# Optimization experiments

Measured on AMD Instinct MI355X. Metric: run time of the kernel, lower is better.

Reference implementation:

```python
import jax, jax.numpy as jnp
import numpy as np

NUM_SPIXELS = 256
N_ITER = 3
TEMP = 1.0


def setup_inputs() -> dict:
    key = jax.random.key(0)
    features = jax.random.normal(key, (4, 16, 256, 256), dtype=jnp.float32)
    return {"features": features}


def reference(features):
    B, C, H, W = features.shape
    dt = features.dtype
    # torch.linspace(0, h-1, h)/h == arange(h)/h
    y = jnp.arange(H, dtype=dt) / H
    x = jnp.arange(W, dtype=dt) / W
    mesh_y, mesh_x = jnp.meshgrid(y, x, indexing='ij')  # each [H, W]
    xy = jnp.stack([mesh_x, mesh_y], axis=0)            # [2, H, W]
    xy_b = jnp.broadcast_to(xy, (B, 2, H, W))

    pixel = jnp.concatenate([features, xy_b], axis=1).reshape(B, C + 2, H * W)
    p = pixel.transpose(0, 2, 1)  # [B, N, D], D = C+2

    s = max(1, int(NUM_SPIXELS ** 0.5))
    # adaptive_avg_pool2d to (s, s); H, W divisible by s -> exact block mean
    def pool(t):
        D = t.shape[1]
        return t.reshape(B, D, s, H // s, s, W // s).mean(axis=(3, 5)).reshape(B, D, s * s)

    centers = jnp.concatenate([pool(features), pool(xy_b)], axis=1)  # [B, D, M]
    c = centers.transpose(0, 2, 1)  # [B, M, D]

    Q = None
    for i in range(N_ITER):
        # Euclidean cdist: ||p||^2 + ||c||^2 - 2 p.c, clipped and sqrt'ed
        d2 = (jnp.sum(p * p, axis=-1)[:, :, None]
              + jnp.sum(c * c, axis=-1)[:, None, :]
              - 2.0 * jnp.einsum('bnd,bmd->bnm', p, c))
        dist = jnp.sqrt(jnp.maximum(d2, 1e-12))  # [B, N, M]
        Q = jax.nn.softmax(-dist * TEMP, axis=-1)
        if i < N_ITER - 1:
            norm = jnp.sum(Q, axis=1)[:, :, None] + 1e-6        # [B, M, 1]
            c = jnp.einsum('bnm,bnd->bmd', Q, p) / norm         # [B, M, D]

    centers_feat = c[:, :, :C].transpose(0, 2, 1)  # [B, C, M]
    return Q, centers_feat
```

## Files before the change

### kernel.cpp

```cpp
#include <hip/hip_runtime.h>
#include <hip/hip_bf16.h>
#include <math.h>

#define BB 4
#define CC 16
#define HH 256
#define WW 256
#define NN (HH*WW)
#define MM 256
#define CROW 20
#define PROW 20
#define PIX 32
#define TSUB 4
#define PIXPERBLK (PIX*TSUB)
#define CHUNKS (NN/PIXPERBLK)

typedef float f32x2 __attribute__((ext_vector_type(2)));
typedef float f32x4v __attribute__((ext_vector_type(4)));
typedef short bf16x8 __attribute__((ext_vector_type(8)));

__device__ __forceinline__ f32x2 mk2(float a, float b) { f32x2 r; r.x = a; r.y = b; return r; }
__device__ __forceinline__ f32x2 pk_fma(f32x2 a, f32x2 b, f32x2 c) {
    return __builtin_elementwise_fma(a, b, c);
}

__device__ __forceinline__ short bfhi(float f, float& hif) {
    __hip_bfloat16 h = __float2bfloat16(f);
    hif = __bfloat162float(h);
    return __builtin_bit_cast(short, h);
}
__device__ __forceinline__ short bflo(float f, float hif) {
    __hip_bfloat16 l = __float2bfloat16(f - hif);
    return __builtin_bit_cast(short, l);
}

__global__ void init_centers(const float* __restrict__ feat, float* __restrict__ cbuf)
{
    const int b    = blockIdx.x >> 8;
    const int m    = blockIdx.x & 255;
    const int lane = threadIdx.x;
    const int sy = m >> 4, sx = m & 15;

    float cvals[16];
#pragma unroll
    for (int d = 0; d < 16; ++d) {
        float v = 0.f;
#pragma unroll
        for (int k = 0; k < 4; ++k) {
            int q  = lane + (k << 6);
            int py = q >> 4, px = q & 15;
            int n  = (sy*16 + py)*WW + sx*16 + px;
            v += feat[((b*CC + d) << 16) + n];
        }
#pragma unroll
        for (int off = 32; off; off >>= 1) v += __shfl_down(v, off);
        cvals[d] = v * (1.f/256.f);
    }
    if (lane == 0) {
        float* row = cbuf + (b*MM + m)*CROW;
        float cn2 = 0.f;
#pragma unroll
        for (int d = 0; d < 16; ++d) { row[d] = cvals[d]; cn2 = fmaf(cvals[d], cvals[d], cn2); }
        float cx = (sx*16 + 7.5f) * (1.f/256.f);
        float cy = (sy*16 + 7.5f) * (1.f/256.f);
        row[16] = cx; row[17] = cy;
        cn2 = fmaf(cx, cx, cn2);
        cn2 = fmaf(cy, cy, cn2);
        row[18] = cn2;
        row[19] = 0.f;
    }
}

__global__ void build_pt(const float* __restrict__ feat, float* __restrict__ ptbuf)
{
    const int b = blockIdx.x >> 8;
    const int n = ((blockIdx.x & 255) << 8) | threadIdx.x;
    float v[16];
#pragma unroll
    for (int d = 0; d < 16; ++d) v[d] = feat[((b*CC + d) << 16) + n];
    float x = (float)(n & 255) * (1.f/256.f);
    float y = (float)(n >> 8) * (1.f/256.f);
    float pn2 = 0.f;
#pragma unroll
    for (int d = 0; d < 16; ++d) pn2 = fmaf(v[d], v[d], pn2);
    pn2 = fmaf(x, x, pn2);
    pn2 = fmaf(y, y, pn2);
    float4* row = reinterpret_cast<float4*>(ptbuf + (size_t)(b*NN + n)*PROW);
    row[0] = make_float4(v[0],  v[1],  v[2],  v[3]);
    row[1] = make_float4(v[4],  v[5],  v[6],  v[7]);
    row[2] = make_float4(v[8],  v[9],  v[10], v[11]);
    row[3] = make_float4(v[12], v[13], v[14], v[15]);
    row[4] = make_float4(x, y, pn2, 1.0f);
}

__global__ __launch_bounds__(256, 3)
void ssn_nf(const float* __restrict__ ptbuf, const float* __restrict__ cbuf,
            float* __restrict__ pp)
{
    __shared__ __align__(16) float pls[PIXPERBLK*PROW];
    __shared__ float ssum_s[4][32];
    __shared__ float w_s[32];

    const int tid    = threadIdx.x;
    const int b      = blockIdx.x >> 9;
    const int chunk  = blockIdx.x & (CHUNKS-1);
    const int n_base = chunk * PIXPERBLK;
    const int L      = tid & 63;
    const int wv     = tid >> 6;
    const int g      = L >> 4;
    const int al     = L & 15;

    {
        const float4* src = reinterpret_cast<const float4*>(
            ptbuf + (size_t)(b*NN + n_base)*PROW);
#pragma unroll
        for (int k = 0; k < 3; ++k) {
            int f = tid + (k << 8);
            if (f < PIXPERBLK*PROW/4)
                reinterpret_cast<float4*>(pls)[f] = src[f];
        }
    }

    bf16x8 bhi[4], blo[4]; float cn2m[4];
#pragma unroll
    for (int mt = 0; mt < 4; ++mt) {
        const float* crow = cbuf + (size_t)(b*MM + wv*64 + mt*16 + al)*CROW;
        float bf_[8];
#pragma unroll
        for (int j = 0; j < 8; ++j) bf_[j] = 0.f;
        if (g < 2) {
            float4 c0 = *reinterpret_cast<const float4*>(crow + 8*g);
            float4 c1 = *reinterpret_cast<const float4*>(crow + 8*g + 4);
            bf_[0]=c0.x; bf_[1]=c0.y; bf_[2]=c0.z; bf_[3]=c0.w;
            bf_[4]=c1.x; bf_[5]=c1.y; bf_[6]=c1.z; bf_[7]=c1.w;
        } else if (g == 2) {
            float4 c0 = *reinterpret_cast<const float4*>(crow + 16);
            bf_[0]=c0.x; bf_[1]=c0.y;
        }
#pragma unroll
        for (int j = 0; j < 8; ++j) {
            float hf;
            bhi[mt][j] = bfhi(bf_[j], hf);
            blo[mt][j] = bflo(bf_[j], hf);
        }
        cn2m[mt] = crow[18];
    }

    f32x4v accA[4], accB[4];
#pragma unroll
    for (int mt = 0; mt < 4; ++mt) {
        accA[mt] = (f32x4v){0.f,0.f,0.f,0.f};
        accB[mt] = (f32x4v){0.f,0.f,0.f,0.f};
    }

    __syncthreads();

#pragma unroll
    for (int pair = 0; pair < 4; ++pair) {
        const int pxt = pair*32;
        float e[2][4][4];
        float part[2][4];

#pragma unroll
        for (int h = 0; h < 2; ++h) {
            const int pxb = pxt + h*16;
            float af[8];
#pragma unroll
            for (int j = 0; j < 8; ++j) af[j] = 0.f;
            const int abase = (pxb + al)*PROW;
            if (g < 2) {
                float4 x0 = *reinterpret_cast<const float4*>(&pls[abase + 8*g]);
                float4 x1 = *reinterpret_cast<const float4*>(&pls[abase + 8*g + 4]);
                af[0]=x0.x; af[1]=x0.y; af[2]=x0.z; af[3]=x0.w;
                af[4]=x1.x; af[5]=x1.y; af[6]=x1.z; af[7]=x1.w;
            } else if (g == 2) {
                float4 x0 = *reinterpret_cast<const float4*>(&pls[abase + 16]);
                af[0]=x0.x; af[1]=x0.y;
            }
            bf16x8 ahi, alo;
#pragma unroll
            for (int j = 0; j < 8; ++j) {
                float hf;
                ahi[j] = bfhi(af[j], hf);
                alo[j] = bflo(af[j], hf);
            }

            float pn2v[4];
#pragma unroll
            for (int r = 0; r < 4; ++r)
                pn2v[r] = pls[(pxb + 4*g + r)*PROW + 18];

#pragma unroll
            for (int mt = 0; mt < 4; ++mt) {
                f32x4v dt = {0.f, 0.f, 0.f, 0.f};
                dt = __builtin_amdgcn_mfma_f32_16x16x32_bf16(ahi, bhi[mt], dt, 0, 0, 0);
                dt = __builtin_amdgcn_mfma_f32_16x16x32_bf16(ahi, blo[mt], dt, 0, 0, 0);
                dt = __builtin_amdgcn_mfma_f32_16x16x32_bf16(alo, bhi[mt], dt, 0, 0, 0);
#pragma unroll
                for (int r = 0; r < 4; ++r) {
                    float d2 = fmaf(-2.f, dt[r], pn2v[r] + cn2m[mt]);
                    e[h][mt][r] = __expf(-__builtin_amdgcn_sqrtf(fmaxf(d2, 1e-12f)));
                }
            }
#pragma unroll
            for (int r = 0; r < 4; ++r)
                part[h][r] = (e[h][0][r] + e[h][1][r]) + (e[h][2][r] + e[h][3][r]);
        }

#pragma unroll
        for (int mask = 1; mask <= 8; mask <<= 1) {
#pragma unroll
            for (int h = 0; h < 2; ++h)
#pragma unroll
                for (int r = 0; r < 4; ++r)
                    part[h][r] += __shfl_xor(part[h][r], mask);
        }
        if (al == 0) {
#pragma unroll
            for (int h = 0; h < 2; ++h)
#pragma unroll
                for (int r = 0; r < 4; ++r)
                    ssum_s[wv][h*16 + 4*g + r] = part[h][r];
        }
        __syncthreads();
        if (tid < 32)
            w_s[tid] = 1.0f / (ssum_s[0][tid] + ssum_s[1][tid]
                             + ssum_s[2][tid] + ssum_s[3][tid]);
        __syncthreads();

        float w0[4], w1[4];
#pragma unroll
        for (int r = 0; r < 4; ++r) {
            w0[r] = w_s[4*g + r];
            w1[r] = w_s[16 + 4*g + r];
        }

        bf16x8 p0h, p0l, p1h, p1l;
#pragma unroll
        for (int j = 0; j < 8; ++j) {
            const int px = pxt + ((j < 4) ? (4*g + j) : (16 + 4*g + (j-4)));
            float f0 = pls[px*PROW + al];
            float h0f;
            p0h[j] = bfhi(f0, h0f);
            p0l[j] = bflo(f0, h0f);
            float f1 = (al < 4) ? pls[px*PROW + 16 + al] : 0.f;
            float h1f;
            p1h[j] = bfhi(f1, h1f);
            p1l[j] = bflo(f1, h1f);
        }

#pragma unroll
        for (int mt = 0; mt < 4; ++mt) {
            bf16x8 awh, awl;
#pragma unroll
            for (int j = 0; j < 8; ++j) {
                float ev = (j < 4) ? e[0][mt][j] * w0[j]
                                   : e[1][mt][j-4] * w1[j-4];
                float hf;
                awh[j] = bfhi(ev, hf);
                awl[j] = bflo(ev, hf);
            }
            accA[mt] = __builtin_amdgcn_mfma_f32_16x16x32_bf16(awh, p0h, accA[mt], 0, 0, 0);
            accA[mt] = __builtin_amdgcn_mfma_f32_16x16x32_bf16(awh, p0l, accA[mt], 0, 0, 0);
            accA[mt] = __builtin_amdgcn_mfma_f32_16x16x32_bf16(awl, p0h, accA[mt], 0, 0, 0);
            accB[mt] = __builtin_amdgcn_mfma_f32_16x16x32_bf16(awh, p1h, accB[mt], 0, 0, 0);
            accB[mt] = __builtin_amdgcn_mfma_f32_16x16x32_bf16(awh, p1l, accB[mt], 0, 0, 0);
            accB[mt] = __builtin_amdgcn_mfma_f32_16x16x32_bf16(awl, p1h, accB[mt], 0, 0, 0);
        }
    }

#pragma unroll
    for (int mt = 0; mt < 4; ++mt) {
#pragma unroll
        for (int r = 0; r < 4; ++r) {
            const int m = wv*64 + mt*16 + 4*g + r;
            float* dst = pp + ((size_t)(b*CHUNKS + chunk)*MM + m)*PROW;
            dst[al] = accA[mt][r];
            if (al < 4) dst[16 + al] = accB[mt][r];
        }
    }
}

__device__ __forceinline__ void rowdot4(const float* __restrict__ prow,
                                        const f32x2 (&cp)[4][9], const float (&cn2)[4],
                                        float (&e)[4])
{
    const float4* pv = reinterpret_cast<const float4*>(prow);
    float4 q0 = pv[0], q1 = pv[1], q2 = pv[2], q3 = pv[3], q4 = pv[4];
    f32x2 u[9];
    u[0]=mk2(q0.x,q0.y); u[1]=mk2(q0.z,q0.w); u[2]=mk2(q1.x,q1.y);
    u[3]=mk2(q1.z,q1.w); u[4]=mk2(q2.x,q2.y); u[5]=mk2(q2.z,q2.w);
    u[6]=mk2(q3.x,q3.y); u[7]=mk2(q3.z,q3.w); u[8]=mk2(q4.x,q4.y);
    f32x2 d0=mk2(0.f,0.f), d1=mk2(0.f,0.f), d2=mk2(0.f,0.f), d3=mk2(0.f,0.f);
#pragma unroll
    for (int i = 0; i < 9; ++i) {
        d0 = pk_fma(u[i], cp[0][i], d0);
        d1 = pk_fma(u[i], cp[1][i], d1);
        d2 = pk_fma(u[i], cp[2][i], d2);
        d3 = pk_fma(u[i], cp[3][i], d3);
    }
    float s0 = fmaf(-2.f, d0.x + d0.y, q4.z + cn2[0]);
    float s1 = fmaf(-2.f, d1.x + d1.y, q4.z + cn2[1]);
    float s2 = fmaf(-2.f, d2.x + d2.y, q4.z + cn2[2]);
    float s3 = fmaf(-2.f, d3.x + d3.y, q4.z + cn2[3]);
    e[0] = __expf(-__builtin_amdgcn_sqrtf(fmaxf(s0, 1e-12f)));
    e[1] = __expf(-__builtin_amdgcn_sqrtf(fmaxf(s1, 1e-12f)));
    e[2] = __expf(-__builtin_amdgcn_sqrtf(fmaxf(s2, 1e-12f)));
    e[3] = __expf(-__builtin_amdgcn_sqrtf(fmaxf(s3, 1e-12f)));
}

#define RS8(L, s) \
    { const bool hi = ((L) & 1); \
      _Pragma("unroll") for (int k = 0; k < 4; ++k) { \
        float a = s[k], bq = s[k+4]; \
        float recv = __shfl_xor(hi ? a : bq, 1); \
        s[k] = (hi ? bq : a) + recv; } } \
    { const bool hi = ((L) & 2); \
      _Pragma("unroll") for (int k = 0; k < 2; ++k) { \
        float a = s[k], bq = s[k+2]; \
        float recv = __shfl_xor(hi ? a : bq, 2); \
        s[k] = (hi ? bq : a) + recv; } } \
    { const bool hi = ((L) & 4); \
      { float a = s[0], bq = s[1]; \
        float recv = __shfl_xor(hi ? a : bq, 4); \
        s[0] = (hi ? bq : a) + recv; } } \
    s[0] += __shfl_xor(s[0], 8); \
    s[0] += __shfl_xor(s[0], 16); \
    s[0] += __shfl_xor(s[0], 32);

__global__ __launch_bounds__(256, 3)
void ssn_fin(const float* __restrict__ ptbuf, const float* __restrict__ cbuf,
             float* __restrict__ qout)
{
    __shared__ __align__(16) float pls[PIXPERBLK*PROW];

    const int tid    = threadIdx.x;
    const int b      = blockIdx.x >> 9;
    const int chunk  = blockIdx.x & (CHUNKS-1);
    const int n_base = chunk * PIXPERBLK;
    const int L      = tid & 63;
    const int wv     = tid >> 6;

    {
        const float4* src = reinterpret_cast<const float4*>(
            ptbuf + (size_t)(b*NN + n_base)*PROW);
#pragma unroll
        for (int k = 0; k < 3; ++k) {
            int f = tid + (k << 8);
            if (f < PIXPERBLK*PROW/4)
                reinterpret_cast<float4*>(pls)[f] = src[f];
        }
    }

    f32x2 cp[4][9]; float cn2[4];
#pragma unroll
    for (int j = 0; j < 4; ++j) {
        const float4* cv = reinterpret_cast<const float4*>(
            cbuf + (b*MM + 4*L + j)*CROW);
        float4 a0 = cv[0], a1 = cv[1], a2 = cv[2], a3 = cv[3], a4 = cv[4];
        cp[j][0]=mk2(a0.x,a0.y); cp[j][1]=mk2(a0.z,a0.w);
        cp[j][2]=mk2(a1.x,a1.y); cp[j][3]=mk2(a1.z,a1.w);
        cp[j][4]=mk2(a2.x,a2.y); cp[j][5]=mk2(a2.z,a2.w);
        cp[j][6]=mk2(a3.x,a3.y); cp[j][7]=mk2(a3.z,a3.w);
        cp[j][8]=mk2(a4.x,a4.y); cn2[j]=a4.z;
    }

    __syncthreads();

    for (int t = 0; t < TSUB; ++t) {
        const int pxb = t*PIX + wv*8;

        float e[4][8];
        float s[8];
#pragma unroll
        for (int k = 0; k < 8; ++k) {
            float ek[4];
            rowdot4(&pls[(pxb + k)*PROW], cp, cn2, ek);
            e[0][k] = ek[0]; e[1][k] = ek[1]; e[2][k] = ek[2]; e[3][k] = ek[3];
            s[k] = (ek[0] + ek[1]) + (ek[2] + ek[3]);
        }

        RS8(L, s)
        float wr = 1.0f / s[0];
        float w[8];
#pragma unroll
        for (int k = 0; k < 8; ++k)
            w[k] = __shfl(wr, ((k&1)<<2) | (k&2) | ((k>>2)&1));

#pragma unroll
        for (int k = 0; k < 8; ++k) {
            size_t rowoff = ((size_t)(b*NN + n_base + pxb + k)) << 8;
            float4 qv = make_float4(e[0][k]*w[k], e[1][k]*w[k],
                                    e[2][k]*w[k], e[3][k]*w[k]);
            *reinterpret_cast<float4*>(qout + rowoff + 4*L) = qv;
        }
    }
}

__global__ __launch_bounds__(256)
void reduce_finalize(const float* __restrict__ pp, float* __restrict__ cbuf,
                     float* __restrict__ cfout, int write_cf)
{
    const int b   = blockIdx.x >> 8;
    const int m   = blockIdx.x & 255;
    const int tid = threadIdx.x;
    const int lane = tid & 63, wv = tid >> 6;

    const float4* r0 = reinterpret_cast<const float4*>(
        pp + ((size_t)(b*CHUNKS + tid)*MM + m)*PROW);
    const float4* r1 = reinterpret_cast<const float4*>(
        pp + ((size_t)(b*CHUNKS + tid + 256)*MM + m)*PROW);
    float a[20];
    {
        float4 u0=r0[0], u1=r0[1], u2=r0[2], u3=r0[3], u4=r0[4];
        float4 w0=r1[0], w1=r1[1], w2=r1[2], w3=r1[3], w4=r1[4];
        a[0]=u0.x+w0.x;  a[1]=u0.y+w0.y;  a[2]=u0.z+w0.z;  a[3]=u0.w+w0.w;
        a[4]=u1.x+w1.x;  a[5]=u1.y+w1.y;  a[6]=u1.z+w1.z;  a[7]=u1.w+w1.w;
        a[8]=u2.x+w2.x;  a[9]=u2.y+w2.y;  a[10]=u2.z+w2.z; a[11]=u2.w+w2.w;
        a[12]=u3.x+w3.x; a[13]=u3.y+w3.y; a[14]=u3.z+w3.z; a[15]=u3.w+w3.w;
        a[16]=u4.x+w4.x; a[17]=u4.y+w4.y; a[18]=u4.z+w4.z; a[19]=u4.w+w4.w;
    }
#pragma unroll
    for (int off = 32; off; off >>= 1) {
#pragma unroll
        for (int d = 0; d < 20; ++d) a[d] += __shfl_down(a[d], off);
    }

    __shared__ float red[4][20];
    if (lane == 0) {
#pragma unroll
        for (int d = 0; d < 20; ++d) red[wv][d] = a[d];
    }
    __syncthreads();
    if (tid == 0) {
        float s[20];
#pragma unroll
        for (int d = 0; d < 20; ++d)
            s[d] = red[0][d] + red[1][d] + red[2][d] + red[3][d];
        float den = s[19] + 1e-6f;
        float* row = cbuf + (b*MM + m)*CROW;
        float cn2 = 0.f;
#pragma unroll
        for (int d = 0; d < 18; ++d) {
            float cv = s[d] / den;
            row[d] = cv;
            cn2 = fmaf(cv, cv, cn2);
            if (write_cf && d < 16) cfout[((b*CC + d) << 8) + m] = cv;
        }
        row[18] = cn2;
        row[19] = 0.f;
    }
}

extern "C" void kernel_launch(void* const* d_in, const int* in_sizes, int n_in,
                              void* d_out, int out_size, void* d_ws, size_t ws_size,
                              hipStream_t stream)
{
    const float* feat = (const float*)d_in[0];
    float* dout = (float*)d_out;

    float* cbuf  = (float*)d_ws;
    float* ptbuf = cbuf + 32768;
    float* pp    = ptbuf + (size_t)BB*NN*PROW;

    float* qout  = dout;
    float* cfout = dout + (size_t)BB*NN*MM;

    build_pt<<<dim3(BB*256), dim3(256), 0, stream>>>(feat, ptbuf);
    init_centers<<<dim3(BB*MM), dim3(64), 0, stream>>>(feat, cbuf);

    for (int it = 0; it < 2; ++it) {
        ssn_nf<<<dim3(BB*CHUNKS), dim3(256), 0, stream>>>(ptbuf, cbuf, pp);
        reduce_finalize<<<dim3(BB*MM), dim3(256), 0, stream>>>(pp, cbuf, cfout, it == 1);
    }
    ssn_fin<<<dim3(BB*CHUNKS), dim3(256), 0, stream>>>(ptbuf, cbuf, qout);
}
```

Baseline: 229.4 us.

## Compute final-pass distances in ssn_fin with split-bf16 MFMA instead of packed FMA

The final Q kernel now computes pixel-center dot products with 16x16x32 bf16 MFMA, using a hi/lo bf16 split (three MFMAs) to keep near-fp32 accuracy, in place of per-lane packed fp32 FMAs. Work is re-partitioned so each wave owns 64 centers and processes 32 pixels at a time. Row sums for the softmax are reduced across waves through shared memory with two added barriers per step. Occupancy hint rises from 3 to 4 blocks. Q stores become scalar 4-byte writes with 16-lane contiguity rather than float4 writes, and the bf16 split introduces small numerical error.

```diff
diff --git a/kernel.cpp b/kernel.cpp
--- a/kernel.cpp
+++ b/kernel.cpp
@@ -15,14 +15,8 @@
 #define PIXPERBLK (PIX*TSUB)
 #define CHUNKS (NN/PIXPERBLK)
 
-typedef float f32x2 __attribute__((ext_vector_type(2)));
 typedef float f32x4v __attribute__((ext_vector_type(4)));
 typedef short bf16x8 __attribute__((ext_vector_type(8)));
-
-__device__ __forceinline__ f32x2 mk2(float a, float b) { f32x2 r; r.x = a; r.y = b; return r; }
-__device__ __forceinline__ f32x2 pk_fma(f32x2 a, f32x2 b, f32x2 c) {
-    return __builtin_elementwise_fma(a, b, c);
-}
 
 __device__ __forceinline__ short bfhi(float f, float& hif) {
     __hip_bfloat16 h = __float2bfloat16(f);
@@ -281,58 +275,13 @@
     }
 }
 
-__device__ __forceinline__ void rowdot4(const float* __restrict__ prow,
-                                        const f32x2 (&cp)[4][9], const float (&cn2)[4],
-                                        float (&e)[4])
-{
-    const float4* pv = reinterpret_cast<const float4*>(prow);
-    float4 q0 = pv[0], q1 = pv[1], q2 = pv[2], q3 = pv[3], q4 = pv[4];
-    f32x2 u[9];
-    u[0]=mk2(q0.x,q0.y); u[1]=mk2(q0.z,q0.w); u[2]=mk2(q1.x,q1.y);
-    u[3]=mk2(q1.z,q1.w); u[4]=mk2(q2.x,q2.y); u[5]=mk2(q2.z,q2.w);
-    u[6]=mk2(q3.x,q3.y); u[7]=mk2(q3.z,q3.w); u[8]=mk2(q4.x,q4.y);
-    f32x2 d0=mk2(0.f,0.f), d1=mk2(0.f,0.f), d2=mk2(0.f,0.f), d3=mk2(0.f,0.f);
-#pragma unroll
-    for (int i = 0; i < 9; ++i) {
-        d0 = pk_fma(u[i], cp[0][i], d0);
-        d1 = pk_fma(u[i], cp[1][i], d1);
-        d2 = pk_fma(u[i], cp[2][i], d2);
-        d3 = pk_fma(u[i], cp[3][i], d3);
-    }
-    float s0 = fmaf(-2.f, d0.x + d0.y, q4.z + cn2[0]);
-    float s1 = fmaf(-2.f, d1.x + d1.y, q4.z + cn2[1]);
-    float s2 = fmaf(-2.f, d2.x + d2.y, q4.z + cn2[2]);
-    float s3 = fmaf(-2.f, d3.x + d3.y, q4.z + cn2[3]);
-    e[0] = __expf(-__builtin_amdgcn_sqrtf(fmaxf(s0, 1e-12f)));
-    e[1] = __expf(-__builtin_amdgcn_sqrtf(fmaxf(s1, 1e-12f)));
-    e[2] = __expf(-__builtin_amdgcn_sqrtf(fmaxf(s2, 1e-12f)));
-    e[3] = __expf(-__builtin_amdgcn_sqrtf(fmaxf(s3, 1e-12f)));
-}
-
-#define RS8(L, s) \
-    { const bool hi = ((L) & 1); \
-      _Pragma("unroll") for (int k = 0; k < 4; ++k) { \
-        float a = s[k], bq = s[k+4]; \
-        float recv = __shfl_xor(hi ? a : bq, 1); \
-        s[k] = (hi ? bq : a) + recv; } } \
-    { const bool hi = ((L) & 2); \
-      _Pragma("unroll") for (int k = 0; k < 2; ++k) { \
-        float a = s[k], bq = s[k+2]; \
-        float recv = __shfl_xor(hi ? a : bq, 2); \
-        s[k] = (hi ? bq : a) + recv; } } \
-    { const bool hi = ((L) & 4); \
-      { float a = s[0], bq = s[1]; \
-        float recv = __shfl_xor(hi ? a : bq, 4); \
-        s[0] = (hi ? bq : a) + recv; } } \
-    s[0] += __shfl_xor(s[0], 8); \
-    s[0] += __shfl_xor(s[0], 16); \
-    s[0] += __shfl_xor(s[0], 32);
-
-__global__ __launch_bounds__(256, 3)
+__global__ __launch_bounds__(256, 4)
 void ssn_fin(const float* __restrict__ ptbuf, const float* __restrict__ cbuf,
              float* __restrict__ qout)
 {
     __shared__ __align__(16) float pls[PIXPERBLK*PROW];
+    __shared__ float ssum_s[4][32];
+    __shared__ float w_s[32];
 
     const int tid    = threadIdx.x;
     const int b      = blockIdx.x >> 9;
@@ -340,6 +289,8 @@
     const int n_base = chunk * PIXPERBLK;
     const int L      = tid & 63;
     const int wv     = tid >> 6;
+    const int g      = L >> 4;
+    const int al     = L & 15;
 
     {
         const float4* src = reinterpret_cast<const float4*>(
@@ -352,47 +303,117 @@
         }
     }
 
-    f32x2 cp[4][9]; float cn2[4];
-#pragma unroll
-    for (int j = 0; j < 4; ++j) {
-        const float4* cv = reinterpret_cast<const float4*>(
-            cbuf + (b*MM + 4*L + j)*CROW);
-        float4 a0 = cv[0], a1 = cv[1], a2 = cv[2], a3 = cv[3], a4 = cv[4];
-        cp[j][0]=mk2(a0.x,a0.y); cp[j][1]=mk2(a0.z,a0.w);
-        cp[j][2]=mk2(a1.x,a1.y); cp[j][3]=mk2(a1.z,a1.w);
-        cp[j][4]=mk2(a2.x,a2.y); cp[j][5]=mk2(a2.z,a2.w);
-        cp[j][6]=mk2(a3.x,a3.y); cp[j][7]=mk2(a3.z,a3.w);
-        cp[j][8]=mk2(a4.x,a4.y); cn2[j]=a4.z;
+    bf16x8 bhi[4], blo[4]; float cn2m[4];
+#pragma unroll
+    for (int mt = 0; mt < 4; ++mt) {
+        const float* crow = cbuf + (size_t)(b*MM + wv*64 + mt*16 + al)*CROW;
+        float bf_[8];
+#pragma unroll
+        for (int j = 0; j < 8; ++j) bf_[j] = 0.f;
+        if (g < 2) {
+            float4 c0 = *reinterpret_cast<const float4*>(crow + 8*g);
+            float4 c1 = *reinterpret_cast<const float4*>(crow + 8*g + 4);
+            bf_[0]=c0.x; bf_[1]=c0.y; bf_[2]=c0.z; bf_[3]=c0.w;
+            bf_[4]=c1.x; bf_[5]=c1.y; bf_[6]=c1.z; bf_[7]=c1.w;
+        } else if (g == 2) {
+            float4 c0 = *reinterpret_cast<const float4*>(crow + 16);
+            bf_[0]=c0.x; bf_[1]=c0.y;
+        }
+#pragma unroll
+        for (int j = 0; j < 8; ++j) {
+            float hf;
+            bhi[mt][j] = bfhi(bf_[j], hf);
+            blo[mt][j] = bflo(bf_[j], hf);
+        }
+        cn2m[mt] = crow[18];
     }
 
     __syncthreads();
 
-    for (int t = 0; t < TSUB; ++t) {
-        const int pxb = t*PIX + wv*8;
-
-        float e[4][8];
-        float s[8];
-#pragma unroll
-        for (int k = 0; k < 8; ++k) {
-            float ek[4];
-            rowdot4(&pls[(pxb + k)*PROW], cp, cn2, ek);
-            e[0][k] = ek[0]; e[1][k] = ek[1]; e[2][k] = ek[2]; e[3][k] = ek[3];
-            s[k] = (ek[0] + ek[1]) + (ek[2] + ek[3]);
-        }
-
-        RS8(L, s)
-        float wr = 1.0f / s[0];
-        float w[8];
-#pragma unroll
-        for (int k = 0; k < 8; ++k)
-            w[k] = __shfl(wr, ((k&1)<<2) | (k&2) | ((k>>2)&1));
-
-#pragma unroll
-        for (int k = 0; k < 8; ++k) {
-            size_t rowoff = ((size_t)(b*NN + n_base + pxb + k)) << 8;
-            float4 qv = make_float4(e[0][k]*w[k], e[1][k]*w[k],
-                                    e[2][k]*w[k], e[3][k]*w[k]);
-            *reinterpret_cast<float4*>(qout + rowoff + 4*L) = qv;
+#pragma unroll
+    for (int pair = 0; pair < 4; ++pair) {
+        float e[2][4][4];
+        float part[2][4];
+
+#pragma unroll
+        for (int h = 0; h < 2; ++h) {
+            const int pxt = pair*32 + h*16;
+
+            float af[8];
+#pragma unroll
+            for (int j = 0; j < 8; ++j) af[j] = 0.f;
+            const int abase = (pxt + al)*PROW;
+            if (g < 2) {
+                float4 x0 = *reinterpret_cast<const float4*>(&pls[abase + 8*g]);
+                float4 x1 = *reinterpret_cast<const float4*>(&pls[abase + 8*g + 4]);
+                af[0]=x0.x; af[1]=x0.y; af[2]=x0.z; af[3]=x0.w;
+                af[4]=x1.x; af[5]=x1.y; af[6]=x1.z; af[7]=x1.w;
+            } else if (g == 2) {
+                float4 x0 = *reinterpret_cast<const float4*>(&pls[abase + 16]);
+                af[0]=x0.x; af[1]=x0.y;
+            }
+            bf16x8 ahi, alo;
+#pragma unroll
+            for (int j = 0; j < 8; ++j) {
+                float hf;
+                ahi[j] = bfhi(af[j], hf);
+                alo[j] = bflo(af[j], hf);
+            }
+
+            float pn2v[4];
+#pragma unroll
+            for (int r = 0; r < 4; ++r)
+                pn2v[r] = pls[(pxt + 4*g + r)*PROW + 18];
+
+#pragma unroll
+            for (int mt = 0; mt < 4; ++mt) {
+                f32x4v dt = {0.f, 0.f, 0.f, 0.f};
+                dt = __builtin_amdgcn_mfma_f32_16x16x32_bf16(ahi, bhi[mt], dt, 0, 0, 0);
+                dt = __builtin_amdgcn_mfma_f32_16x16x32_bf16(ahi, blo[mt], dt, 0, 0, 0);
+                dt = __builtin_amdgcn_mfma_f32_16x16x32_bf16(alo, bhi[mt], dt, 0, 0, 0);
+#pragma unroll
+                for (int r = 0; r < 4; ++r) {
+                    float d2 = fmaf(-2.f, dt[r], pn2v[r] + cn2m[mt]);
+                    e[h][mt][r] = __expf(-__builtin_amdgcn_sqrtf(fmaxf(d2, 1e-12f)));
+                }
+            }
+#pragma unroll
+            for (int r = 0; r < 4; ++r)
+                part[h][r] = (e[h][0][r] + e[h][1][r]) + (e[h][2][r] + e[h][3][r]);
+        }
+
+#pragma unroll
+        for (int mask = 1; mask <= 8; mask <<= 1) {
+#pragma unroll
+            for (int h = 0; h < 2; ++h)
+#pragma unroll
+                for (int r = 0; r < 4; ++r)
+                    part[h][r] += __shfl_xor(part[h][r], mask);
+        }
+        if (al == 0) {
+#pragma unroll
+            for (int h = 0; h < 2; ++h)
+#pragma unroll
+                for (int r = 0; r < 4; ++r)
+                    ssum_s[wv][h*16 + 4*g + r] = part[h][r];
+        }
+        __syncthreads();
+        if (tid < 32)
+            w_s[tid] = 1.0f / (ssum_s[0][tid] + ssum_s[1][tid]
+                             + ssum_s[2][tid] + ssum_s[3][tid]);
+        __syncthreads();
+
+#pragma unroll
+        for (int h = 0; h < 2; ++h) {
+#pragma unroll
+            for (int r = 0; r < 4; ++r) {
+                const float w = w_s[h*16 + 4*g + r];
+                const size_t rowoff =
+                    ((size_t)(b*NN + n_base + pair*32 + h*16 + 4*g + r)) << 8;
+#pragma unroll
+                for (int mt = 0; mt < 4; ++mt)
+                    qout[rowoff + wv*64 + mt*16 + al] = e[h][mt][r] * w;
+            }
         }
     }
 }
```

Result: slower. 234.6 us (+2.3%).
